# Optimization experiments

Hardware: AMD Instinct MI355X
Metric: run time of the kernel (lower is better)

Reference implementation:

```python
import jax, jax.numpy as jnp
import numpy as np

N = 40000          # spots (nodes)
G = 3000           # genes (input features)
C = 20             # num_classes
E = N * 16         # edges (avg degree 16)


def _uniform(key, shape, stdv):
    return jax.random.uniform(key, shape, jnp.float32, -stdv, stdv)


def _linear_params(key, n_in, n_out):
    # torch Linear default init: U(-1/sqrt(in), 1/sqrt(in)); stored as [in, out]
    k1, k2 = jax.random.split(key)
    s = 1.0 / np.sqrt(n_in)
    return _uniform(k1, (n_in, n_out), s), _uniform(k2, (n_out,), s)


def setup_inputs() -> dict:
    key = jax.random.key(0)
    ks = jax.random.split(key, 32)
    x = jax.random.normal(ks[0], (N, G), jnp.float32)
    adj_rows = jax.random.randint(ks[1], (E,), 0, N, jnp.int32)
    adj_cols = jax.random.randint(ks[2], (E,), 0, N, jnp.int32)
    adj_vals = jax.random.uniform(ks[3], (E,), jnp.float32)

    # GCN weights: GraphConvolution init U(-1/sqrt(out), 1/sqrt(out)), no bias
    def gcn_w(k, fi, fo):
        return _uniform(k, (fi, fo), 1.0 / np.sqrt(fo))

    inp = {
        "x": x, "adj_rows": adj_rows, "adj_cols": adj_cols, "adj_vals": adj_vals,
        "W1": gcn_w(ks[4], G, 512), "W2": gcn_w(ks[5], 512, 256),
        "W3": gcn_w(ks[6], 256, 128), "W4": gcn_w(ks[7], 128, 128),
        "W5": gcn_w(ks[8], 128, C),
    }
    # AE linear layers
    for name, (fi, fo), k in [
        ("enc1", (G, 512), ks[9]), ("enc2", (512, 256), ks[10]),
        ("enc3", (256, 128), ks[11]), ("zl", (128, 128), ks[12]),
        ("dec1", (128, 128), ks[13]), ("dec2", (128, 256), ks[14]),
        ("dec3", (256, 512), ks[15]), ("xbar", (512, G), ks[16]),
    ]:
        w, b = _linear_params(k, fi, fo)
        inp[name + "_w"], inp[name + "_b"] = w, b
    # Attention projection vectors (Linear(in_size, 1, bias=False))
    inp["a1"] = _uniform(ks[17], (512,), 1.0 / np.sqrt(512))
    inp["a2"] = _uniform(ks[18], (256,), 1.0 / np.sqrt(256))
    inp["a3"] = _uniform(ks[19], (128,), 1.0 / np.sqrt(128))
    inp["a4"] = _uniform(ks[20], (128,), 1.0 / np.sqrt(128))
    inp["scale"] = jax.random.normal(ks[21], (G,), jnp.float32)
    inp["additive"] = jax.random.normal(ks[22], (G,), jnp.float32)
    return inp


def _spmm(rows, cols, vals, dense, n):
    # out[r] = sum_e vals[e] * dense[cols[e]] for rows[e]==r  (sparse [n,n] @ dense)
    return jax.ops.segment_sum(vals[:, None] * dense[cols], rows, num_segments=n)


def _gcn(x, rows, cols, vals, W, n, active=True):
    out = _spmm(rows, cols, vals, x @ W, n)
    return jax.nn.relu(out) if active else out


def _attn(h, t, a):
    # stack two [N,D] branches, softmax over the branch axis, weighted sum
    z = jnp.stack([h, t], axis=1)           # [N,2,D]
    w = jnp.einsum('nbd,d->nb', z, a)        # [N,2]
    beta = jax.nn.softmax(w, axis=1)
    return jnp.einsum('nb,nbd->nd', beta, z)


def reference(x, adj_rows, adj_cols, adj_vals,
              W1, W2, W3, W4, W5,
              enc1_w, enc1_b, enc2_w, enc2_b, enc3_w, enc3_b, zl_w, zl_b,
              dec1_w, dec1_b, dec2_w, dec2_b, dec3_w, dec3_b, xbar_w, xbar_b,
              a1, a2, a3, a4, scale, additive):
    n = x.shape[0]
    # autoencoder
    t1 = jax.nn.relu(x @ enc1_w + enc1_b)
    t2 = jax.nn.relu(t1 @ enc2_w + enc2_b)
    t3 = jax.nn.relu(t2 @ enc3_w + enc3_b)
    z = t3 @ zl_w + zl_b
    d1 = jax.nn.relu(z @ dec1_w + dec1_b)
    d2 = jax.nn.relu(d1 @ dec2_w + dec2_b)
    d3 = jax.nn.relu(d2 @ dec3_w + dec3_b)
    x_bar = d3 @ xbar_w + xbar_b
    # GCN stack with attention-fused AE skip connections
    h = _gcn(x, adj_rows, adj_cols, adj_vals, W1, n)
    emb = _attn(h, t1, a1)
    h = _gcn(emb, adj_rows, adj_cols, adj_vals, W2, n)
    emb = _attn(h, t2, a2)
    h = _gcn(emb, adj_rows, adj_cols, adj_vals, W3, n)
    emb = _attn(h, t3, a3)
    h = _gcn(emb, adj_rows, adj_cols, adj_vals, W4, n)
    emb = _attn(h, z, a4)
    output = _gcn(emb, adj_rows, adj_cols, adj_vals, W5, n, active=False)
    return output, x_bar, jax.nn.sigmoid(scale), jnp.exp(additive)
```

## Files before the change

### kernel.cpp

```cpp
#include <hip/hip_runtime.h>
#include <cmath>

typedef unsigned short u16;
typedef unsigned int u32;
typedef __attribute__((ext_vector_type(8))) short short8;
typedef __attribute__((ext_vector_type(4))) short short4v;
typedef __attribute__((ext_vector_type(4))) float f32x4;

__device__ __forceinline__ float bf2f(u16 h) {
  union { u32 u; float f; } v; v.u = ((u32)h) << 16; return v.f;
}
__device__ __forceinline__ u16 f2bf(float f) {
  union { float f; u32 u; } v; v.f = f;
  u32 u = v.u;
  u32 r = (u + 0x7FFFu + ((u >> 16) & 1u)) >> 16;
  return (u16)r;
}

__global__ void convx_kernel(const float* __restrict__ x, u16* __restrict__ A0) {
  int idx = blockIdx.x * 256 + threadIdx.x;
  int r = blockIdx.y;
  if (idx >= 752) return;
  short4v o;
  if (r < 40000 && idx < 750) {
    float4 v = *(const float4*)(x + (size_t)r * 3000 + idx * 4);
    o[0] = (short)f2bf(v.x); o[1] = (short)f2bf(v.y);
    o[2] = (short)f2bf(v.z); o[3] = (short)f2bf(v.w);
  } else {
    o[0] = 0; o[1] = 0; o[2] = 0; o[3] = 0;
  }
  *(short4v*)(A0 + (size_t)r * 3008 + idx * 4) = o;
}

__global__ void convw_kernel(const float* __restrict__ W, u16* __restrict__ Wt,
                             int K, int N, int Kp) {
  int k = blockIdx.x * 256 + threadIdx.x;
  int n = blockIdx.y;
  if (k >= Kp) return;
  float v = (k < K && n < N) ? W[(size_t)k * N + n] : 0.f;
  Wt[(size_t)n * Kp + k] = f2bf(v);
}

__global__ void zero_kernel(int* p, int n) {
  int i = blockIdx.x * 256 + threadIdx.x;
  if (i < n) p[i] = 0;
}
__global__ void count_kernel(const int* __restrict__ rows, int* __restrict__ counts, int E) {
  int i = blockIdx.x * 256 + threadIdx.x;
  if (i < E) atomicAdd(&counts[rows[i]], 1);
}
__global__ __launch_bounds__(1024) void scan_kernel(const int* __restrict__ counts,
                                                    int* __restrict__ rowptr,
                                                    int* __restrict__ cursor, int n) {
  __shared__ int buf[1024];
  __shared__ int carry_s;
  int tid = threadIdx.x;
  if (tid == 0) carry_s = 0;
  __syncthreads();
  for (int base = 0; base < n; base += 1024) {
    int i = base + tid;
    int v = (i < n) ? counts[i] : 0;
    buf[tid] = v;
    __syncthreads();
    for (int off = 1; off < 1024; off <<= 1) {
      int tv = (tid >= off) ? buf[tid - off] : 0;
      __syncthreads();
      buf[tid] += tv;
      __syncthreads();
    }
    int incl = buf[tid];
    int carry = carry_s;
    if (i < n) { int ex = carry + incl - v; rowptr[i] = ex; cursor[i] = ex; }
    __syncthreads();
    if (tid == 1023) carry_s = carry + incl;
    __syncthreads();
  }
  if (tid == 0) rowptr[n] = carry_s;
}
__global__ void scatter_kernel(const int* __restrict__ rows, const int* __restrict__ cols,
                               const float* __restrict__ vals, int* __restrict__ cursor,
                               int* __restrict__ cols_s, float* __restrict__ vals_s, int E) {
  int i = blockIdx.x * 256 + threadIdx.x;
  if (i < E) {
    int r = rows[i];
    int p = atomicAdd(&cursor[r], 1);
    cols_s[p] = cols[i];
    vals_s[p] = vals[i];
  }
}

#define BM 128
#define BN 128
#define BK 32

template <bool BIAS, bool RELU, bool OUTBF16, bool SPLIT, int CH>
__global__ __launch_bounds__(256, 2) void gemm_bf16(
    const u16* __restrict__ A, int lda, const u16* __restrict__ Bt, int ldb,
    void* __restrict__ C1, void* __restrict__ C2, int ldc,
    const float* __restrict__ bias, int M, int Nreal, int K, int MT, int NT) {
  __shared__ __align__(16) u16 As[2][BM * BK];
  __shared__ __align__(16) u16 Bs[2][BN * BK];
  const int lin = blockIdx.x;
  const int per = CH * NT;
  const int g = lin / per;
  const int r0 = lin - g * per;
  const int bx0 = g * CH;
  const int cw = min(CH, MT - bx0);
  const int bx = bx0 + r0 % cw;
  const int by = r0 / cw;

  const int tid = threadIdx.x;
  const int lane = tid & 63;
  const int wave = tid >> 6;
  const int mblk = bx * BM;
  const int nblk = by * BN;
  const int wm = (wave & 1) * 64;
  const int wn = (wave >> 1) * 64;
  const int ml = lane & 15;
  const int kg = lane >> 4;

  f32x4 acc[4][4];
#pragma unroll
  for (int i = 0; i < 4; ++i)
#pragma unroll
    for (int j = 0; j < 4; ++j) acc[i][j] = (f32x4)(0.f);

  const int nk = K / BK;
  const int sr = tid >> 2;
  const int sc = (tid & 3) * 8;
  const u16* gA0 = A + (size_t)(mblk + sr) * lda + sc;
  const u16* gA1 = A + (size_t)(mblk + sr + 64) * lda + sc;
  const u16* gB0 = Bt + (size_t)(nblk + sr) * ldb + sc;
  const u16* gB1 = Bt + (size_t)(nblk + sr + 64) * ldb + sc;

  auto stage = [&](int buf, int kt) {
    const int ko = kt * BK;
    u16* lA = &As[buf][0] + wave * 512;
    u16* lB = &Bs[buf][0] + wave * 512;
    __builtin_amdgcn_global_load_lds((const void*)(gA0 + ko), (void*)lA, 16, 0, 0);
    __builtin_amdgcn_global_load_lds((const void*)(gA1 + ko), (void*)(lA + 2048), 16, 0, 0);
    __builtin_amdgcn_global_load_lds((const void*)(gB0 + ko), (void*)lB, 16, 0, 0);
    __builtin_amdgcn_global_load_lds((const void*)(gB1 + ko), (void*)(lB + 2048), 16, 0, 0);
  };

  stage(0, 0);
  asm volatile("s_waitcnt vmcnt(0)" ::: "memory");
  __syncthreads();

  int cur = 0;
  for (int kt = 0; kt < nk; ++kt) {
    if (kt + 1 < nk) stage(cur ^ 1, kt + 1);
    short8 af[4], bfr[4];
#pragma unroll
    for (int i = 0; i < 4; ++i) {
      af[i] = *(const short8*)&As[cur][(wm + i * 16 + ml) * BK + kg * 8];
      bfr[i] = *(const short8*)&Bs[cur][(wn + i * 16 + ml) * BK + kg * 8];
    }
#pragma unroll
    for (int i = 0; i < 4; ++i)
#pragma unroll
      for (int j = 0; j < 4; ++j)
        acc[i][j] = __builtin_amdgcn_mfma_f32_16x16x32_bf16(af[i], bfr[j], acc[i][j], 0, 0, 0);
    asm volatile("s_waitcnt vmcnt(0)" ::: "memory");
    __syncthreads();
    cur ^= 1;
  }

  const bool second = SPLIT && (nblk >= 512);
#pragma unroll
  for (int i = 0; i < 4; ++i) {
    const int row0 = mblk + wm + i * 16 + kg * 4;
#pragma unroll
    for (int j = 0; j < 4; ++j) {
      const int col = nblk + wn + j * 16 + ml;
      if (col < Nreal) {
        float bv = 0.f;
        if (SPLIT) { if (!second) bv = bias[col]; }
        else if (BIAS) bv = bias[col];
#pragma unroll
        for (int r = 0; r < 4; ++r) {
          const int row = row0 + r;
          if (row < M) {
            float v = acc[i][j][r] + bv;
            if (SPLIT) {
              if (!second) v = fmaxf(v, 0.f);
              u16* dst = second ? (u16*)C2 : (u16*)C1;
              dst[(size_t)row * ldc + (second ? col - 512 : col)] = f2bf(v);
            } else {
              if (RELU) v = fmaxf(v, 0.f);
              if (OUTBF16)
                ((u16*)C1)[(size_t)row * ldc + col] = f2bf(v);
              else
                ((float*)C1)[(size_t)row * ldc + col] = v;
            }
          }
        }
      }
    }
  }
}

template <int D, bool RELU>
__global__ __launch_bounds__(256) void spmm_vec(const int* __restrict__ rowptr,
                                                const int* __restrict__ colidx,
                                                const float* __restrict__ vals,
                                                const u16* __restrict__ X,
                                                u16* __restrict__ Y) {
  constexpr int VE = D / 64;
  const int wave = threadIdx.x >> 6, lane = threadIdx.x & 63;
  const int row = blockIdx.x * 4 + wave;
  const int co = lane * VE;
  float acc[VE];
#pragma unroll
  for (int j = 0; j < VE; ++j) acc[j] = 0.f;
  const int s = rowptr[row], e = rowptr[row + 1];
  for (int i = s; i < e; ++i) {
    const int c = colidx[i];
    const float v = vals[i];
    const u16* xr = X + (size_t)c * D + co;
    if constexpr (VE == 8) {
      short8 x8 = *(const short8*)xr;
#pragma unroll
      for (int j = 0; j < 8; ++j) acc[j] += v * bf2f((u16)x8[j]);
    } else if constexpr (VE == 4) {
      short4v x4 = *(const short4v*)xr;
#pragma unroll
      for (int j = 0; j < 4; ++j) acc[j] += v * bf2f((u16)x4[j]);
    } else {
      u32 x2 = *(const u32*)xr;
      acc[0] += v * bf2f((u16)(x2 & 0xffffu));
      acc[1] += v * bf2f((u16)(x2 >> 16));
    }
  }
  u16* yr = Y + (size_t)row * D + co;
  if constexpr (VE == 8) {
    short8 o;
#pragma unroll
    for (int j = 0; j < 8; ++j) { float f = RELU ? fmaxf(acc[j], 0.f) : acc[j]; o[j] = (short)f2bf(f); }
    *(short8*)yr = o;
  } else if constexpr (VE == 4) {
    short4v o;
#pragma unroll
    for (int j = 0; j < 4; ++j) { float f = RELU ? fmaxf(acc[j], 0.f) : acc[j]; o[j] = (short)f2bf(f); }
    *(short4v*)yr = o;
  } else {
    float f0 = RELU ? fmaxf(acc[0], 0.f) : acc[0];
    float f1 = RELU ? fmaxf(acc[1], 0.f) : acc[1];
    *(u32*)yr = (u32)f2bf(f0) | ((u32)f2bf(f1) << 16);
  }
}

__global__ __launch_bounds__(64) void spmm_out_kernel(const int* __restrict__ rowptr,
                                                      const int* __restrict__ colidx,
                                                      const float* __restrict__ vals,
                                                      const u16* __restrict__ X,
                                                      float* __restrict__ Y) {
  int row = blockIdx.x;
  int c = threadIdx.x;
  float acc = 0.f;
  int s = rowptr[row], e = rowptr[row + 1];
  for (int i = s; i < e; ++i) {
    int col = colidx[i];
    float v = vals[i];
    if (c < 20) acc += v * bf2f(X[(size_t)col * 20 + c]);
  }
  if (c < 20) Y[(size_t)row * 20 + c] = acc;
}

template <int D>
__global__ __launch_bounds__(256) void attn_vec(const u16* __restrict__ h,
                                                const u16* __restrict__ t,
                                                const float* __restrict__ a,
                                                u16* __restrict__ emb) {
  constexpr int VE = D / 64;
  const int wave = threadIdx.x >> 6, lane = threadIdx.x & 63;
  const int row = blockIdx.x * 4 + wave;
  const int co = lane * VE;
  const u16* hr = h + (size_t)row * D + co;
  const u16* tr = t + (size_t)row * D + co;
  float hv[VE], tv[VE];
  if constexpr (VE == 8) {
    short8 h8 = *(const short8*)hr, t8 = *(const short8*)tr;
#pragma unroll
    for (int j = 0; j < 8; ++j) { hv[j] = bf2f((u16)h8[j]); tv[j] = bf2f((u16)t8[j]); }
  } else if constexpr (VE == 4) {
    short4v h4 = *(const short4v*)hr, t4 = *(const short4v*)tr;
#pragma unroll
    for (int j = 0; j < 4; ++j) { hv[j] = bf2f((u16)h4[j]); tv[j] = bf2f((u16)t4[j]); }
  } else {
    u32 h2 = *(const u32*)hr, t2 = *(const u32*)tr;
    hv[0] = bf2f((u16)(h2 & 0xffffu)); hv[1] = bf2f((u16)(h2 >> 16));
    tv[0] = bf2f((u16)(t2 & 0xffffu)); tv[1] = bf2f((u16)(t2 >> 16));
  }
  float wh = 0.f, wt = 0.f;
#pragma unroll
  for (int j = 0; j < VE; ++j) {
    float av = a[co + j];
    wh += av * hv[j];
    wt += av * tv[j];
  }
  for (int off = 32; off; off >>= 1) {
    wh += __shfl_xor(wh, off);
    wt += __shfl_xor(wt, off);
  }
  float m = fmaxf(wh, wt);
  float e1 = expf(wh - m), e2 = expf(wt - m);
  float inv = 1.f / (e1 + e2);
  float b1 = e1 * inv, b2 = e2 * inv;
  u16* er = emb + (size_t)row * D + co;
  if constexpr (VE == 8) {
    short8 o;
#pragma unroll
    for (int j = 0; j < 8; ++j) o[j] = (short)f2bf(b1 * hv[j] + b2 * tv[j]);
    *(short8*)er = o;
  } else if constexpr (VE == 4) {
    short4v o;
#pragma unroll
    for (int j = 0; j < 4; ++j) o[j] = (short)f2bf(b1 * hv[j] + b2 * tv[j]);
    *(short4v*)er = o;
  } else {
    *(u32*)er = (u32)f2bf(b1 * hv[0] + b2 * tv[0]) | ((u32)f2bf(b1 * hv[1] + b2 * tv[1]) << 16);
  }
}

__global__ __launch_bounds__(64) void xw5_kernel(const u16* __restrict__ emb,
                                                 const float* __restrict__ W5,
                                                 u16* __restrict__ xw5) {
  int row = blockIdx.x;
  int c = threadIdx.x;
  if (c >= 20) return;
  const short8* er = (const short8*)(emb + (size_t)row * 128);
  float acc = 0.f;
#pragma unroll
  for (int k8 = 0; k8 < 16; ++k8) {
    short8 v = er[k8];
#pragma unroll
    for (int j = 0; j < 8; ++j) acc += bf2f((u16)v[j]) * W5[(k8 * 8 + j) * 20 + c];
  }
  xw5[(size_t)row * 20 + c] = f2bf(acc);
}

__global__ void sig_exp_kernel(const float* __restrict__ scale, const float* __restrict__ additive,
                               float* __restrict__ osig, float* __restrict__ oexp, int g) {
  int i = blockIdx.x * 256 + threadIdx.x;
  if (i < g) {
    osig[i] = 1.f / (1.f + expf(-scale[i]));
    oexp[i] = expf(additive[i]);
  }
}

extern "C" void kernel_launch(void* const* d_in, const int* in_sizes, int n_in,
                              void* d_out, int out_size, void* d_ws, size_t ws_size,
                              hipStream_t stream) {
  (void)n_in; (void)out_size; (void)ws_size;
  const float* x      = (const float*)d_in[0];
  const int*   arows  = (const int*)d_in[1];
  const int*   acols  = (const int*)d_in[2];
  const float* avals  = (const float*)d_in[3];
  const float* W1     = (const float*)d_in[4];
  const float* W2     = (const float*)d_in[5];
  const float* W3     = (const float*)d_in[6];
  const float* W4     = (const float*)d_in[7];
  const float* W5     = (const float*)d_in[8];
  const float* enc1_w = (const float*)d_in[9],  *enc1_b = (const float*)d_in[10];
  const float* enc2_w = (const float*)d_in[11], *enc2_b = (const float*)d_in[12];
  const float* enc3_w = (const float*)d_in[13], *enc3_b = (const float*)d_in[14];
  const float* zl_w   = (const float*)d_in[15], *zl_b   = (const float*)d_in[16];
  const float* dec1_w = (const float*)d_in[17], *dec1_b = (const float*)d_in[18];
  const float* dec2_w = (const float*)d_in[19], *dec2_b = (const float*)d_in[20];
  const float* dec3_w = (const float*)d_in[21], *dec3_b = (const float*)d_in[22];
  const float* xbar_w = (const float*)d_in[23], *xbar_b = (const float*)d_in[24];
  const float* a1 = (const float*)d_in[25], *a2 = (const float*)d_in[26];
  const float* a3 = (const float*)d_in[27], *a4 = (const float*)d_in[28];
  const float* scale = (const float*)d_in[29], *additive = (const float*)d_in[30];

  const int E = in_sizes[1];
  const int N = 40000, G = 3000, Kx = 3008, Mp = 40064;

  float* out      = (float*)d_out;
  float* out_gcn  = out;
  float* out_xbar = out + (size_t)N * 20;
  float* out_sig  = out_xbar + (size_t)N * G;
  float* out_exp  = out_sig + G;

  char* wsb = (char*)d_ws;
  size_t off = 0;
  auto alloc = [&](size_t b) -> void* {
    void* p = wsb + off;
    off = (off + b + 255) & ~(size_t)255;
    return p;
  };
  u16* A0    = (u16*)alloc((size_t)Mp * Kx * 2);
  u16* t1    = (u16*)alloc((size_t)Mp * 512 * 2);
  u16* t2    = (u16*)alloc((size_t)Mp * 256 * 2);
  u16* t3    = (u16*)alloc((size_t)Mp * 128 * 2);
  u16* zb    = (u16*)alloc((size_t)Mp * 128 * 2);
  u16* dd1   = (u16*)alloc((size_t)Mp * 128 * 2);
  u16* dd2   = (u16*)alloc((size_t)Mp * 256 * 2);
  u16* dd3   = (u16*)alloc((size_t)Mp * 512 * 2);
  u16* xw    = (u16*)alloc((size_t)Mp * 512 * 2);
  u16* hb    = (u16*)alloc((size_t)Mp * 512 * 2);
  u16* emb   = (u16*)alloc((size_t)Mp * 512 * 2);
  u16* xw5   = (u16*)alloc((size_t)N * 20 * 2);
  u16* catT  = (u16*)alloc((size_t)1024 * Kx * 2);
  u16* enc2T = (u16*)alloc((size_t)256 * 512 * 2);
  u16* enc3T = (u16*)alloc((size_t)128 * 256 * 2);
  u16* zlT   = (u16*)alloc((size_t)128 * 128 * 2);
  u16* dec1T = (u16*)alloc((size_t)128 * 128 * 2);
  u16* dec2T = (u16*)alloc((size_t)256 * 128 * 2);
  u16* dec3T = (u16*)alloc((size_t)512 * 256 * 2);
  u16* xbarT = (u16*)alloc((size_t)3072 * 512 * 2);
  u16* W2T   = (u16*)alloc((size_t)256 * 512 * 2);
  u16* W3T   = (u16*)alloc((size_t)128 * 256 * 2);
  u16* W4T   = (u16*)alloc((size_t)128 * 128 * 2);
  int* counts = (int*)alloc((size_t)N * 4);
  int* rowptr = (int*)alloc((size_t)(N + 1) * 4);
  int* cursor = (int*)alloc((size_t)N * 4);
  int* colss  = (int*)alloc((size_t)E * 4);
  float* valss = (float*)alloc((size_t)E * 4);

  convx_kernel<<<dim3(3, Mp), 256, 0, stream>>>(x, A0);
  auto convw = [&](const float* W, u16* Wt, int K, int Nw, int Kp, int Np) {
    convw_kernel<<<dim3((Kp + 255) / 256, Np), 256, 0, stream>>>(W, Wt, K, Nw, Kp);
  };
  convw(enc1_w, catT,             3000, 512, Kx, 512);
  convw(W1,     catT + 512 * Kx,  3000, 512, Kx, 512);
  convw(enc2_w, enc2T, 512, 256, 512, 256);
  convw(enc3_w, enc3T, 256, 128, 256, 128);
  convw(zl_w,   zlT,   128, 128, 128, 128);
  convw(dec1_w, dec1T, 128, 128, 128, 128);
  convw(dec2_w, dec2T, 128, 256, 128, 256);
  convw(dec3_w, dec3T, 256, 512, 256, 512);
  convw(xbar_w, xbarT, 512, 3000, 512, 3072);
  convw(W2,     W2T,   512, 256, 512, 256);
  convw(W3,     W3T,   256, 128, 256, 128);
  convw(W4,     W4T,   128, 128, 128, 128);

  zero_kernel<<<(N + 255) / 256, 256, 0, stream>>>(counts, N);
  count_kernel<<<(E + 255) / 256, 256, 0, stream>>>(arows, counts, E);
  scan_kernel<<<1, 1024, 0, stream>>>(counts, rowptr, cursor, N);
  scatter_kernel<<<(E + 255) / 256, 256, 0, stream>>>(arows, acols, avals, cursor, colss, valss, E);

  const int MT = 313;
  gemm_bf16<false, false, true, true, 32><<<MT * 8, 256, 0, stream>>>(
      A0, Kx, catT, Kx, t1, xw, 512, enc1_b, N, 1024, Kx, MT, 8);
  gemm_bf16<true, true, true, false, 32><<<MT * 2, 256, 0, stream>>>(
      t1, 512, enc2T, 512, t2, nullptr, 256, enc2_b, N, 256, 512, MT, 2);
  gemm_bf16<true, true, true, false, 32><<<MT * 1, 256, 0, stream>>>(
      t2, 256, enc3T, 256, t3, nullptr, 128, enc3_b, N, 128, 256, MT, 1);
  gemm_bf16<true, false, true, false, 32><<<MT * 1, 256, 0, stream>>>(
      t3, 128, zlT, 128, zb, nullptr, 128, zl_b, N, 128, 128, MT, 1);
  gemm_bf16<true, true, true, false, 32><<<MT * 1, 256, 0, stream>>>(
      zb, 128, dec1T, 128, dd1, nullptr, 128, dec1_b, N, 128, 128, MT, 1);
  gemm_bf16<true, true, true, false, 32><<<MT * 2, 256, 0, stream>>>(
      dd1, 128, dec2T, 128, dd2, nullptr, 256, dec2_b, N, 256, 128, MT, 2);
  gemm_bf16<true, true, true, false, 32><<<MT * 4, 256, 0, stream>>>(
      dd2, 256, dec3T, 256, dd3, nullptr, 512, dec3_b, N, 512, 256, MT, 4);
  gemm_bf16<true, false, false, false, 32><<<MT * 24, 256, 0, stream>>>(
      dd3, 512, xbarT, 512, out_xbar, nullptr, 3000, xbar_b, N, 3000, 512, MT, 24);

  spmm_vec<512, true><<<N / 4, 256, 0, stream>>>(rowptr, colss, valss, xw, hb);
  attn_vec<512><<<N / 4, 256, 0, stream>>>(hb, t1, a1, emb);
  gemm_bf16<false, false, true, false, 32><<<MT * 2, 256, 0, stream>>>(
      emb, 512, W2T, 512, xw, nullptr, 256, nullptr, N, 256, 512, MT, 2);
  spmm_vec<256, true><<<N / 4, 256, 0, stream>>>(rowptr, colss, valss, xw, hb);
  attn_vec<256><<<N / 4, 256, 0, stream>>>(hb, t2, a2, emb);
  gemm_bf16<false, false, true, false, 32><<<MT * 1, 256, 0, stream>>>(
      emb, 256, W3T, 256, xw, nullptr, 128, nullptr, N, 128, 256, MT, 1);
  spmm_vec<128, true><<<N / 4, 256, 0, stream>>>(rowptr, colss, valss, xw, hb);
  attn_vec<128><<<N / 4, 256, 0, stream>>>(hb, t3, a3, emb);
  gemm_bf16<false, false, true, false, 32><<<MT * 1, 256, 0, stream>>>(
      emb, 128, W4T, 128, xw, nullptr, 128, nullptr, N, 128, 128, MT, 1);
  spmm_vec<128, true><<<N / 4, 256, 0, stream>>>(rowptr, colss, valss, xw, hb);
  attn_vec<128><<<N / 4, 256, 0, stream>>>(hb, zb, a4, emb);

  xw5_kernel<<<N, 64, 0, stream>>>(emb, W5, xw5);
  spmm_out_kernel<<<N, 64, 0, stream>>>(rowptr, colss, valss, xw5, out_gcn);

  sig_exp_kernel<<<(G + 255) / 256, 256, 0, stream>>>(scale, additive, out_sig, out_exp, G);
}
```

Before: 1.505 ms.

## Add 256x256 swizzled LDS-DMA GEMM for the two large GEMMs

Adds a new 512-thread GEMM kernel with 256x256 output tiles and BK=64. It stages tiles through direct global-to-LDS loads into XOR-swizzled shared memory, double-buffered, with loads interleaved into the MFMA phases and raised wave priority. The kernel replaces the 128x128 GEMM for the x@[enc1|W1] product and the x_bar decoder GEMM, aiming for more data reuse per loaded byte and better overlap of memory with compute. Padded row count grows to 40192 so full 256-row tiles can be read; the xbar path relies on padded weight columns, and the larger tile and LDS footprint lower occupancy.

```diff
diff --git a/kernel.cpp b/kernel.cpp
--- a/kernel.cpp
+++ b/kernel.cpp
@@ -93,10 +93,10 @@
 #define BN 128
 #define BK 32
 
-template <bool BIAS, bool RELU, bool OUTBF16, bool SPLIT, int CH>
+template <bool BIAS, bool RELU, bool OUTBF16, int CH>
 __global__ __launch_bounds__(256, 2) void gemm_bf16(
     const u16* __restrict__ A, int lda, const u16* __restrict__ Bt, int ldb,
-    void* __restrict__ C1, void* __restrict__ C2, int ldc,
+    void* __restrict__ C1, int ldc,
     const float* __restrict__ bias, int M, int Nreal, int K, int MT, int NT) {
   __shared__ __align__(16) u16 As[2][BM * BK];
   __shared__ __align__(16) u16 Bs[2][BN * BK];
@@ -166,7 +166,6 @@
     cur ^= 1;
   }
 
-  const bool second = SPLIT && (nblk >= 512);
 #pragma unroll
   for (int i = 0; i < 4; ++i) {
     const int row0 = mblk + wm + i * 16 + kg * 4;
@@ -174,25 +173,162 @@
     for (int j = 0; j < 4; ++j) {
       const int col = nblk + wn + j * 16 + ml;
       if (col < Nreal) {
-        float bv = 0.f;
-        if (SPLIT) { if (!second) bv = bias[col]; }
-        else if (BIAS) bv = bias[col];
+        float bv = BIAS ? bias[col] : 0.f;
 #pragma unroll
         for (int r = 0; r < 4; ++r) {
           const int row = row0 + r;
           if (row < M) {
             float v = acc[i][j][r] + bv;
-            if (SPLIT) {
-              if (!second) v = fmaxf(v, 0.f);
-              u16* dst = second ? (u16*)C2 : (u16*)C1;
-              dst[(size_t)row * ldc + (second ? col - 512 : col)] = f2bf(v);
-            } else {
-              if (RELU) v = fmaxf(v, 0.f);
-              if (OUTBF16)
-                ((u16*)C1)[(size_t)row * ldc + col] = f2bf(v);
-              else
-                ((float*)C1)[(size_t)row * ldc + col] = v;
-            }
+            if (RELU) v = fmaxf(v, 0.f);
+            if (OUTBF16)
+              ((u16*)C1)[(size_t)row * ldc + col] = f2bf(v);
+            else
+              ((float*)C1)[(size_t)row * ldc + col] = v;
+          }
+        }
+      }
+    }
+  }
+}
+
+template <int MODE>
+__global__ __launch_bounds__(512, 1) void gemm256(
+    const u16* __restrict__ A, int lda, const u16* __restrict__ Bt, int ldb,
+    void* __restrict__ C1, void* __restrict__ C2, int ldc,
+    const float* __restrict__ bias, int M, int Nreal, int K, int NT) {
+  __shared__ __align__(16) u16 lds[2][2][256 * 64];
+  const int tid = threadIdx.x;
+  const int lane = tid & 63;
+  const int wave = tid >> 6;
+  const int wm = wave >> 2;
+  const int wn = wave & 3;
+  const int ml = lane & 15;
+  const int kg = lane >> 4;
+
+  const int bx = blockIdx.x / NT;
+  const int by = blockIdx.x % NT;
+  const int mblk = bx * 256;
+  const int nblk = by * 256;
+
+  f32x4 acc[8][4];
+#pragma unroll
+  for (int i = 0; i < 8; ++i)
+#pragma unroll
+    for (int j = 0; j < 4; ++j) acc[i][j] = (f32x4)(0.f);
+
+  const int srow = tid >> 3;
+  const int clog = (tid & 7) ^ (srow & 7);
+  const size_t abase = (size_t)(mblk + srow) * lda + clog * 8;
+  const size_t bbase = (size_t)(nblk + srow) * ldb + clog * 8;
+  const int NKT = K / 64;
+
+  auto stageA = [&](int d, int kt, int h) {
+    u16* dst = &lds[d][0][0] + h * 4096 + wave * 512;
+    const u16* src = A + abase + (size_t)h * 64 * lda + kt * 64;
+    __builtin_amdgcn_global_load_lds((const void*)src, (void*)dst, 16, 0, 0);
+  };
+  auto stageB = [&](int d, int kt, int h) {
+    u16* dst = &lds[d][1][0] + h * 4096 + wave * 512;
+    const u16* src = Bt + bbase + (size_t)h * 64 * ldb + kt * 64;
+    __builtin_amdgcn_global_load_lds((const void*)src, (void*)dst, 16, 0, 0);
+  };
+  auto stagePair = [&](int d, int kt, int q) {
+    if (q == 0)      { stageB(d, kt, 0); stageB(d, kt, 1); }
+    else if (q == 1) { stageB(d, kt, 2); stageB(d, kt, 3); }
+    else if (q == 2) { stageA(d, kt, 0); stageA(d, kt, 2); }
+    else             { stageA(d, kt, 1); stageA(d, kt, 3); }
+  };
+  auto readA = [&](int d, int im, int kk) -> short8 {
+    const int r = wm * 128 + im * 16 + ml;
+    const int ch = (kk * 4 + kg) ^ (r & 7);
+    return *(const short8*)&lds[d][0][r * 64 + ch * 8];
+  };
+  auto readB = [&](int d, int j, int kk) -> short8 {
+    const int r = wn * 64 + j * 16 + ml;
+    const int ch = (kk * 4 + kg) ^ (r & 7);
+    return *(const short8*)&lds[d][1][r * 64 + ch * 8];
+  };
+
+#pragma unroll
+  for (int q = 0; q < 4; ++q) stagePair(0, 0, q);
+  asm volatile("s_waitcnt vmcnt(2)" ::: "memory");
+  __builtin_amdgcn_s_barrier();
+
+  for (int kt = 0; kt < NKT; ++kt) {
+    const int d = kt & 1;
+    const bool more = (kt + 1 < NKT);
+    short8 bf2[4][2];
+#pragma unroll
+    for (int q = 0; q < 4; ++q) {
+      if (q == 0) {
+#pragma unroll
+        for (int j = 0; j < 4; ++j) { bf2[j][0] = readB(d, j, 0); bf2[j][1] = readB(d, j, 1); }
+      }
+      short8 a00 = readA(d, 2 * q, 0);
+      short8 a01 = readA(d, 2 * q, 1);
+      short8 a10 = readA(d, 2 * q + 1, 0);
+      short8 a11 = readA(d, 2 * q + 1, 1);
+      if (more) stagePair(d ^ 1, kt + 1, q);
+      __builtin_amdgcn_s_barrier();
+      asm volatile("s_waitcnt lgkmcnt(0)" ::: "memory");
+      __builtin_amdgcn_s_setprio(1);
+#pragma unroll
+      for (int j = 0; j < 4; ++j) {
+        acc[2 * q][j]     = __builtin_amdgcn_mfma_f32_16x16x32_bf16(a00, bf2[j][0], acc[2 * q][j], 0, 0, 0);
+        acc[2 * q + 1][j] = __builtin_amdgcn_mfma_f32_16x16x32_bf16(a10, bf2[j][0], acc[2 * q + 1][j], 0, 0, 0);
+      }
+#pragma unroll
+      for (int j = 0; j < 4; ++j) {
+        acc[2 * q][j]     = __builtin_amdgcn_mfma_f32_16x16x32_bf16(a01, bf2[j][1], acc[2 * q][j], 0, 0, 0);
+        acc[2 * q + 1][j] = __builtin_amdgcn_mfma_f32_16x16x32_bf16(a11, bf2[j][1], acc[2 * q + 1][j], 0, 0, 0);
+      }
+      __builtin_amdgcn_s_setprio(0);
+      if (q == 1) {
+        if (more) asm volatile("s_waitcnt vmcnt(4)" ::: "memory");
+        else      asm volatile("s_waitcnt vmcnt(0)" ::: "memory");
+      }
+      if (q == 3 && more) asm volatile("s_waitcnt vmcnt(2)" ::: "memory");
+      __builtin_amdgcn_s_barrier();
+    }
+  }
+
+  const int crow0 = mblk + wm * 128;
+  const int ccol0 = nblk + wn * 64;
+  if (MODE == 0) {
+    const bool second = (nblk >= 512);
+#pragma unroll
+    for (int i = 0; i < 8; ++i) {
+      const int row0 = crow0 + i * 16 + kg * 4;
+#pragma unroll
+      for (int j = 0; j < 4; ++j) {
+        const int col = ccol0 + j * 16 + ml;
+        const float bv = second ? 0.f : bias[col];
+#pragma unroll
+        for (int r = 0; r < 4; ++r) {
+          const int row = row0 + r;
+          if (row < M) {
+            float v = acc[i][j][r] + bv;
+            if (!second) v = fmaxf(v, 0.f);
+            u16* dst = second ? (u16*)C2 : (u16*)C1;
+            dst[(size_t)row * 512 + (second ? col - 512 : col)] = f2bf(v);
+          }
+        }
+      }
+    }
+  } else {
+#pragma unroll
+    for (int i = 0; i < 8; ++i) {
+      const int row0 = crow0 + i * 16 + kg * 4;
+#pragma unroll
+      for (int j = 0; j < 4; ++j) {
+        const int col = ccol0 + j * 16 + ml;
+        if (col < Nreal) {
+          const float bv = bias[col];
+#pragma unroll
+          for (int r = 0; r < 4; ++r) {
+            const int row = row0 + r;
+            if (row < M)
+              ((float*)C1)[(size_t)row * ldc + col] = acc[i][j][r] + bv;
           }
         }
       }
@@ -375,7 +511,8 @@
   const float* scale = (const float*)d_in[29], *additive = (const float*)d_in[30];
 
   const int E = in_sizes[1];
-  const int N = 40000, G = 3000, Kx = 3008, Mp = 40064;
+  const int N = 40000, G = 3000, Kx = 3008;
+  const int Mp = 40192;
 
   float* out      = (float*)d_out;
   float* out_gcn  = out;
@@ -442,35 +579,34 @@
   scatter_kernel<<<(E + 255) / 256, 256, 0, stream>>>(arows, acols, avals, cursor, colss, valss, E);
 
   const int MT = 313;
-  gemm_bf16<false, false, true, true, 32><<<MT * 8, 256, 0, stream>>>(
-      A0, Kx, catT, Kx, t1, xw, 512, enc1_b, N, 1024, Kx, MT, 8);
-  gemm_bf16<true, true, true, false, 32><<<MT * 2, 256, 0, stream>>>(
-      t1, 512, enc2T, 512, t2, nullptr, 256, enc2_b, N, 256, 512, MT, 2);
-  gemm_bf16<true, true, true, false, 32><<<MT * 1, 256, 0, stream>>>(
-      t2, 256, enc3T, 256, t3, nullptr, 128, enc3_b, N, 128, 256, MT, 1);
-  gemm_bf16<true, false, true, false, 32><<<MT * 1, 256, 0, stream>>>(
-      t3, 128, zlT, 128, zb, nullptr, 128, zl_b, N, 128, 128, MT, 1);
-  gemm_bf16<true, true, true, false, 32><<<MT * 1, 256, 0, stream>>>(
-      zb, 128, dec1T, 128, dd1, nullptr, 128, dec1_b, N, 128, 128, MT, 1);
-  gemm_bf16<true, true, true, false, 32><<<MT * 2, 256, 0, stream>>>(
-      dd1, 128, dec2T, 128, dd2, nullptr, 256, dec2_b, N, 256, 128, MT, 2);
-  gemm_bf16<true, true, true, false, 32><<<MT * 4, 256, 0, stream>>>(
-      dd2, 256, dec3T, 256, dd3, nullptr, 512, dec3_b, N, 512, 256, MT, 4);
-  gemm_bf16<true, false, false, false, 32><<<MT * 24, 256, 0, stream>>>(
-      dd3, 512, xbarT, 512, out_xbar, nullptr, 3000, xbar_b, N, 3000, 512, MT, 24);
+  const int MT2 = 157;
+  gemm256<0><<<MT2 * 4, 512, 0, stream>>>(A0, Kx, catT, Kx, t1, xw, 512, enc1_b, N, 1024, Kx, 4);
+  gemm_bf16<true, true, true, 32><<<MT * 2, 256, 0, stream>>>(
+      t1, 512, enc2T, 512, t2, 256, enc2_b, N, 256, 512, MT, 2);
+  gemm_bf16<true, true, true, 32><<<MT * 1, 256, 0, stream>>>(
+      t2, 256, enc3T, 256, t3, 128, enc3_b, N, 128, 256, MT, 1);
+  gemm_bf16<true, false, true, 32><<<MT * 1, 256, 0, stream>>>(
+      t3, 128, zlT, 128, zb, 128, zl_b, N, 128, 128, MT, 1);
+  gemm_bf16<true, true, true, 32><<<MT * 1, 256, 0, stream>>>(
+      zb, 128, dec1T, 128, dd1, 128, dec1_b, N, 128, 128, MT, 1);
+  gemm_bf16<true, true, true, 32><<<MT * 2, 256, 0, stream>>>(
+      dd1, 128, dec2T, 128, dd2, 256, dec2_b, N, 256, 128, MT, 2);
+  gemm_bf16<true, true, true, 32><<<MT * 4, 256, 0, stream>>>(
+      dd2, 256, dec3T, 256, dd3, 512, dec3_b, N, 512, 256, MT, 4);
+  gemm256<1><<<MT2 * 12, 512, 0, stream>>>(dd3, 512, xbarT, 512, out_xbar, nullptr, 3000, xbar_b, N, 3000, 512, 12);
 
   spmm_vec<512, true><<<N / 4, 256, 0, stream>>>(rowptr, colss, valss, xw, hb);
   attn_vec<512><<<N / 4, 256, 0, stream>>>(hb, t1, a1, emb);
-  gemm_bf16<false, false, true, false, 32><<<MT * 2, 256, 0, stream>>>(
-      emb, 512, W2T, 512, xw, nullptr, 256, nullptr, N, 256, 512, MT, 2);
+  gemm_bf16<false, false, true, 32><<<MT * 2, 256, 0, stream>>>(
+      emb, 512, W2T, 512, xw, 256, nullptr, N, 256, 512, MT, 2);
   spmm_vec<256, true><<<N / 4, 256, 0, stream>>>(rowptr, colss, valss, xw, hb);
   attn_vec<256><<<N / 4, 256, 0, stream>>>(hb, t2, a2, emb);
-  gemm_bf16<false, false, true, false, 32><<<MT * 1, 256, 0, stream>>>(
-      emb, 256, W3T, 256, xw, nullptr, 128, nullptr, N, 128, 256, MT, 1);
+  gemm_bf16<false, false, true, 32><<<MT * 1, 256, 0, stream>>>(
+      emb, 256, W3T, 256, xw, 128, nullptr, N, 128, 256, MT, 1);
   spmm_vec<128, true><<<N / 4, 256, 0, stream>>>(rowptr, colss, valss, xw, hb);
   attn_vec<128><<<N / 4, 256, 0, stream>>>(hb, t3, a3, emb);
-  gemm_bf16<false, false, true, false, 32><<<MT * 1, 256, 0, stream>>>(
-      emb, 128, W4T, 128, xw, nullptr, 128, nullptr, N, 128, 128, MT, 1);
+  gemm_bf16<false, false, true, 32><<<MT * 1, 256, 0, stream>>>(
+      emb, 128, W4T, 128, xw, 128, nullptr, N, 128, 128, MT, 1);
   spmm_vec<128, true><<<N / 4, 256, 0, stream>>>(rowptr, colss, valss, xw, hb);
   attn_vec<128><<<N / 4, 256, 0, stream>>>(hb, zb, a4, emb);
 
```

New measurement: 1.484 ms. Within noise of the previous version (-1.4%).
